# Kernel optimization log

Hardware: AMD Instinct MI355X
Metric: run time of the kernel (lower is better)

The kernel has to match this reference:

```python
import jax, jax.numpy as jnp
import numpy as np

N_NODES = 50000


def setup_inputs() -> dict:
    key = jax.random.key(0)
    k1, k2, k3, k4, k5, k6 = jax.random.split(key, 6)
    N, T, F_IN, F_OUT, E = N_NODES, 4, 64, 64, 800000
    node_features = jax.random.normal(k1, (N, T, F_IN), dtype=jnp.float32)
    edge_weights = jax.random.uniform(k2, (T, E), dtype=jnp.float32)
    src = jax.random.randint(k3, (E,), 0, N, dtype=jnp.int32)
    dst = jax.random.randint(k4, (E,), 0, N, dtype=jnp.int32)
    weight = jax.random.normal(k5, (F_OUT, F_IN), dtype=jnp.float32) / np.sqrt(F_IN)
    bias = jax.random.normal(k6, (F_OUT,), dtype=jnp.float32) * 0.01
    return {"node_features": node_features, "edge_weights": edge_weights,
            "src": src, "dst": dst, "weight": weight, "bias": bias}


def reference(node_features, edge_weights, src, dst, weight, bias):
    # edge_weights: (T, E) -> per-edge weights (E, T)
    ew = edge_weights.T  # (E, T)
    # gather source node features: (E, T, F); multiply by per-edge/timestep scalar
    msg = ew[:, :, None] * node_features[src]  # (E, T, F)
    # scatter-sum into destination nodes: (N, T, F)
    h = jax.ops.segment_sum(msg, dst, num_segments=N_NODES)
    # final linear: (N, T, F_out)
    out = jnp.einsum('ntf,of->nto', h, weight) + bias
    return out
```

## Files before the change

### kernel.cpp

```cpp
#include <hip/hip_runtime.h>


#define F_DIM 64
#define TF 256

__device__ __forceinline__ unsigned short f2bf(float x) {
  unsigned u = __float_as_uint(x);
  return (unsigned short)((u + 0x7FFF + ((u >> 16) & 1)) >> 16);
}
__device__ __forceinline__ float bf2f(unsigned short b) {
  return __uint_as_float(((unsigned)b) << 16);
}
__device__ __forceinline__ void fma4(float4& a, float s, float4 w) {
  a.x += s * w.x; a.y += s * w.y; a.z += s * w.z; a.w += s * w.w;
}

__global__ __launch_bounds__(256) void hist_kernel(
    const int* __restrict__ dst, int* __restrict__ cnt, int E) {
  int e = blockIdx.x * 256 + threadIdx.x;
  if (e < E) atomicAdd(&cnt[dst[e]], 1);
}

__global__ __launch_bounds__(1024) void scanA_kernel(
    const int* __restrict__ cnt, int* __restrict__ off, int* __restrict__ bsum, int N) {
  __shared__ int wsum[16];
  int tid = threadIdx.x;
  int i = blockIdx.x * 1024 + tid;
  int v = (i < N) ? cnt[i] : 0;
  int lane = tid & 63;
  int incl = v;
  #pragma unroll
  for (int s = 1; s < 64; s <<= 1) {
    int t = __shfl_up(incl, s, 64);
    if (lane >= s) incl += t;
  }
  int w = tid >> 6;
  if (lane == 63) wsum[w] = incl;
  __syncthreads();
  if (w == 0) {
    int x = (lane < 16) ? wsum[lane] : 0;
    #pragma unroll
    for (int s = 1; s < 16; s <<= 1) {
      int t = __shfl_up(x, s, 64);
      if (lane >= s) x += t;
    }
    if (lane < 16) wsum[lane] = x;
  }
  __syncthreads();
  int wpre = (w == 0) ? 0 : wsum[w - 1];
  if (i < N) off[i] = wpre + incl - v;
  if (tid == 1023) bsum[blockIdx.x] = wpre + incl;
}

__global__ __launch_bounds__(64) void scanB_kernel(int* __restrict__ bsum, int nb) {
  int lane = threadIdx.x;
  int v = (lane < nb) ? bsum[lane] : 0;
  int incl = v;
  #pragma unroll
  for (int s = 1; s < 64; s <<= 1) {
    int t = __shfl_up(incl, s, 64);
    if (lane >= s) incl += t;
  }
  if (lane < nb) bsum[lane] = incl - v;
}

__global__ __launch_bounds__(1024) void scanC_kernel(
    int* __restrict__ off, const int* __restrict__ bsum, int N, int E) {
  int i = blockIdx.x * 1024 + threadIdx.x;
  if (i < N) off[i] += bsum[blockIdx.x];
  if (i == N) off[N] = E;
}

__global__ __launch_bounds__(256) void fill_kernel(
    const int* __restrict__ dst, const int* __restrict__ src,
    const float* __restrict__ ew, const int* __restrict__ off,
    int* __restrict__ cnt, uint4* __restrict__ rec, int E) {
  int e = blockIdx.x * 256 + threadIdx.x;
  if (e < E) {
    int d = dst[e];
    int pos = off[d] + atomicSub(&cnt[d], 1) - 1;
    unsigned w0 = f2bf(ew[e]),         w1 = f2bf(ew[E + e]);
    unsigned w2 = f2bf(ew[2 * E + e]), w3 = f2bf(ew[3 * E + e]);
    uint4 r;
    r.x = (unsigned)src[e];
    r.y = (w1 << 16) | w0;
    r.z = (w3 << 16) | w2;
    r.w = 0;
    rec[pos] = r;
  }
}

__global__ __launch_bounds__(256) void transform_kernel(
    const float4* __restrict__ nf4, const float* __restrict__ W,
    unsigned short* __restrict__ nfb, int nrows) {
  __shared__ float Wt[64 * 64];
  __shared__ float rows[128][65];
  int tid = threadIdx.x;
  #pragma unroll
  for (int i = tid; i < 4096; i += 256) Wt[(i & 63) * 64 + (i >> 6)] = W[i];
  int rbase = blockIdx.x * 128;
  int nr = min(128, nrows - rbase);
  for (int i = tid; i < nr * 16; i += 256) {
    int r = i >> 4, q = i & 15;
    float4 v = nf4[(size_t)(rbase + r) * 16 + q];
    rows[r][q * 4 + 0] = v.x; rows[r][q * 4 + 1] = v.y;
    rows[r][q * 4 + 2] = v.z; rows[r][q * 4 + 3] = v.w;
  }
  __syncthreads();

  int oq = tid & 7;
  int r0 = (tid >> 3) * 4;
  float4 acc[4][2];
  #pragma unroll
  for (int j = 0; j < 4; ++j) {
    acc[j][0] = make_float4(0.f, 0.f, 0.f, 0.f);
    acc[j][1] = make_float4(0.f, 0.f, 0.f, 0.f);
  }

  const float4* Wt4 = (const float4*)Wt;
  #pragma unroll 8
  for (int f = 0; f < 64; ++f) {
    float4 w0 = Wt4[f * 16 + oq * 2 + 0];
    float4 w1 = Wt4[f * 16 + oq * 2 + 1];
    #pragma unroll
    for (int j = 0; j < 4; ++j) {
      float rv = rows[r0 + j][f];
      fma4(acc[j][0], rv, w0);
      fma4(acc[j][1], rv, w1);
    }
  }

  int obase = oq * 8;
  #pragma unroll
  for (int j = 0; j < 4; ++j) {
    if (r0 + j < nr) {
      size_t rowoff = (size_t)(rbase + r0 + j) * F_DIM + obase;
      #pragma unroll
      for (int c = 0; c < 2; ++c) {
        float4 a = acc[j][c];
        ushort4 u = make_ushort4(f2bf(a.x), f2bf(a.y), f2bf(a.z), f2bf(a.w));
        *reinterpret_cast<ushort4*>(&nfb[rowoff + c * 4]) = u;
      }
    }
  }
}

__global__ __launch_bounds__(256) void gather_bf16_kernel(
    const ushort4* __restrict__ nfb, const uint4* __restrict__ rec,
    const int* __restrict__ off, const float4* __restrict__ bias4,
    float4* __restrict__ out4, int N) {
  int idx = blockIdx.x * 256 + threadIdx.x;
  int n = idx >> 6;
  if (n >= N) return;
  int r = idx & 63, t = r >> 4, q = r & 15;
  int wsel = t >> 1;
  int wshift = (t & 1) << 4;
  int beg = off[n], end = off[n + 1];
  float4 acc = make_float4(0.f, 0.f, 0.f, 0.f);
  int p = beg;
  for (; p + 4 <= end; p += 4) {
    uint4 r0 = rec[p], r1 = rec[p + 1], r2 = rec[p + 2], r3 = rec[p + 3];
    float w0 = __uint_as_float(((wsel ? r0.z : r0.y) >> wshift) << 16);
    float w1 = __uint_as_float(((wsel ? r1.z : r1.y) >> wshift) << 16);
    float w2 = __uint_as_float(((wsel ? r2.z : r2.y) >> wshift) << 16);
    float w3 = __uint_as_float(((wsel ? r3.z : r3.y) >> wshift) << 16);
    ushort4 v0 = nfb[(size_t)r0.x * 64 + t * 16 + q];
    ushort4 v1 = nfb[(size_t)r1.x * 64 + t * 16 + q];
    ushort4 v2 = nfb[(size_t)r2.x * 64 + t * 16 + q];
    ushort4 v3 = nfb[(size_t)r3.x * 64 + t * 16 + q];
    acc.x += w0 * bf2f(v0.x) + w1 * bf2f(v1.x) + w2 * bf2f(v2.x) + w3 * bf2f(v3.x);
    acc.y += w0 * bf2f(v0.y) + w1 * bf2f(v1.y) + w2 * bf2f(v2.y) + w3 * bf2f(v3.y);
    acc.z += w0 * bf2f(v0.z) + w1 * bf2f(v1.z) + w2 * bf2f(v2.z) + w3 * bf2f(v3.z);
    acc.w += w0 * bf2f(v0.w) + w1 * bf2f(v1.w) + w2 * bf2f(v2.w) + w3 * bf2f(v3.w);
  }
  for (; p < end; ++p) {
    uint4 rr = rec[p];
    float w = __uint_as_float(((wsel ? rr.z : rr.y) >> wshift) << 16);
    ushort4 v = nfb[(size_t)rr.x * 64 + t * 16 + q];
    acc.x += w * bf2f(v.x); acc.y += w * bf2f(v.y);
    acc.z += w * bf2f(v.z); acc.w += w * bf2f(v.w);
  }
  float4 b = bias4[q];
  float4 res = make_float4(acc.x + b.x, acc.y + b.y, acc.z + b.z, acc.w + b.w);
  out4[(size_t)n * 64 + t * 16 + q] = res;
}

__global__ __launch_bounds__(256) void gather_f32_kernel(
    const float4* __restrict__ nf4, const uint4* __restrict__ rec,
    const int* __restrict__ off, float4* __restrict__ h4, int N) {
  int idx = blockIdx.x * 256 + threadIdx.x;
  int n = idx >> 6;
  if (n >= N) return;
  int r = idx & 63, t = r >> 4, q = r & 15;
  int wsel = t >> 1;
  int wshift = (t & 1) << 4;
  int beg = off[n], end = off[n + 1];
  float4 acc = make_float4(0.f, 0.f, 0.f, 0.f);
  for (int p = beg; p < end; ++p) {
    uint4 rr = rec[p];
    float w = __uint_as_float(((wsel ? rr.z : rr.y) >> wshift) << 16);
    float4 v = nf4[(size_t)rr.x * 64 + t * 16 + q];
    acc.x += w * v.x; acc.y += w * v.y; acc.z += w * v.z; acc.w += w * v.w;
  }
  h4[(size_t)n * 64 + t * 16 + q] = acc;
}

__global__ __launch_bounds__(256) void linear_kernel(
    float* __restrict__ h, const float* __restrict__ W,
    const float* __restrict__ bias, int nrows) {
  __shared__ float Wt[64 * 65];
  __shared__ float rows[4][64];
  int tid = threadIdx.x;
  for (int i = tid; i < 4096; i += 256) Wt[(i & 63) * 65 + (i >> 6)] = W[i];
  int rr = tid >> 6, o = tid & 63;
  float b = bias[o];
  int rbase = blockIdx.x * 32;
  for (int r0 = 0; r0 < 32; r0 += 4) {
    int row = rbase + r0 + rr;
    __syncthreads();
    if (row < nrows) rows[rr][o] = h[(size_t)row * F_DIM + o];
    __syncthreads();
    if (row < nrows) {
      float acc = b;
      #pragma unroll
      for (int f = 0; f < 64; ++f) acc += rows[rr][f] * Wt[f * 65 + o];
      h[(size_t)row * F_DIM + o] = acc;
    }
  }
}

extern "C" void kernel_launch(void* const* d_in, const int* in_sizes, int n_in,
                              void* d_out, int out_size, void* d_ws, size_t ws_size,
                              hipStream_t stream) {
  const float* nf   = (const float*)d_in[0];
  const float* ew   = (const float*)d_in[1];
  const int*   src  = (const int*)d_in[2];
  const int*   dst  = (const int*)d_in[3];
  const float* W    = (const float*)d_in[4];
  const float* bias = (const float*)d_in[5];
  float* out = (float*)d_out;

  int E = in_sizes[2];
  int N = out_size / TF;
  int nrows = out_size / F_DIM;
  int nfelems = nrows * F_DIM;

  char* wsb = (char*)d_ws;
  int* cnt  = (int*)wsb;
  int* off  = cnt + N;
  int* bsum = off + (N + 1);
  size_t ofs = ((size_t)(2 * N + 1 + 64) * 4 + 15) & ~(size_t)15;
  uint4* rec = (uint4*)(wsb + ofs);           ofs += (size_t)E * 16;
  ofs = (ofs + 511) & ~(size_t)511;
  unsigned short* nfb = (unsigned short*)(wsb + ofs);
  size_t need_bf16 = ofs + (size_t)nfelems * 2;
  bool use_bf16 = ws_size >= need_bf16;

  (void)hipMemsetAsync(cnt, 0, (size_t)N * sizeof(int), stream);

  int eblk = (E + 255) / 256;
  hist_kernel<<<eblk, 256, 0, stream>>>(dst, cnt, E);

  int sblk = (N + 1023) / 1024;
  scanA_kernel<<<sblk, 1024, 0, stream>>>(cnt, off, bsum, N);
  scanB_kernel<<<1, 64, 0, stream>>>(bsum, sblk);
  scanC_kernel<<<(N + 1024) / 1024, 1024, 0, stream>>>(off, bsum, N, E);

  fill_kernel<<<eblk, 256, 0, stream>>>(dst, src, ew, off, cnt, rec, E);

  int gblk = (N * 64 + 255) / 256;
  if (use_bf16) {
    transform_kernel<<<(nrows + 127) / 128, 256, 0, stream>>>(
        (const float4*)nf, W, nfb, nrows);
    gather_bf16_kernel<<<gblk, 256, 0, stream>>>(
        (const ushort4*)nfb, rec, off, (const float4*)bias, (float4*)out, N);
  } else {
    gather_f32_kernel<<<gblk, 256, 0, stream>>>(
        (const float4*)nf, rec, off, (float4*)out, N);
    linear_kernel<<<(nrows + 31) / 32, 256, 0, stream>>>(out, W, bias, nrows);
  }
}
```

Measured before the change: 192.7 us.

## Fuse histogram into transform, drop scanC, split gather by timestep

```diff
diff --git a/kernel.cpp b/kernel.cpp
--- a/kernel.cpp
+++ b/kernel.cpp
@@ -13,12 +13,6 @@
 }
 __device__ __forceinline__ void fma4(float4& a, float s, float4 w) {
   a.x += s * w.x; a.y += s * w.y; a.z += s * w.z; a.w += s * w.w;
-}
-
-__global__ __launch_bounds__(256) void hist_kernel(
-    const int* __restrict__ dst, int* __restrict__ cnt, int E) {
-  int e = blockIdx.x * 256 + threadIdx.x;
-  if (e < E) atomicAdd(&cnt[dst[e]], 1);
 }
 
 __global__ __launch_bounds__(1024) void scanA_kernel(
@@ -64,21 +58,15 @@
   if (lane < nb) bsum[lane] = incl - v;
 }
 
-__global__ __launch_bounds__(1024) void scanC_kernel(
-    int* __restrict__ off, const int* __restrict__ bsum, int N, int E) {
-  int i = blockIdx.x * 1024 + threadIdx.x;
-  if (i < N) off[i] += bsum[blockIdx.x];
-  if (i == N) off[N] = E;
-}
-
 __global__ __launch_bounds__(256) void fill_kernel(
     const int* __restrict__ dst, const int* __restrict__ src,
     const float* __restrict__ ew, const int* __restrict__ off,
-    int* __restrict__ cnt, uint4* __restrict__ rec, int E) {
+    const int* __restrict__ bsum, int* __restrict__ cnt,
+    uint4* __restrict__ rec, int E) {
   int e = blockIdx.x * 256 + threadIdx.x;
   if (e < E) {
     int d = dst[e];
-    int pos = off[d] + atomicSub(&cnt[d], 1) - 1;
+    int pos = off[d] + bsum[d >> 10] + atomicSub(&cnt[d], 1) - 1;
     unsigned w0 = f2bf(ew[e]),         w1 = f2bf(ew[E + e]);
     unsigned w2 = f2bf(ew[2 * E + e]), w3 = f2bf(ew[3 * E + e]);
     uint4 r;
@@ -90,15 +78,24 @@
   }
 }
 
-__global__ __launch_bounds__(256) void transform_kernel(
+__global__ __launch_bounds__(256) void transform_hist_kernel(
     const float4* __restrict__ nf4, const float* __restrict__ W,
-    unsigned short* __restrict__ nfb, int nrows) {
+    unsigned short* __restrict__ nfb, int nrows,
+    const int* __restrict__ dst, int* __restrict__ cnt, int E, int epb) {
   __shared__ float Wt[64 * 64];
   __shared__ float rows[128][65];
   int tid = threadIdx.x;
+
+  {
+    int e0 = blockIdx.x * epb;
+    int e1 = min(e0 + epb, E);
+    for (int e = e0 + tid; e < e1; e += 256) atomicAdd(&cnt[dst[e]], 1);
+  }
+
   #pragma unroll
   for (int i = tid; i < 4096; i += 256) Wt[(i & 63) * 64 + (i >> 6)] = W[i];
   int rbase = blockIdx.x * 128;
+  if (rbase >= nrows) return;
   int nr = min(128, nrows - rbase);
   for (int i = tid; i < nr * 16; i += 256) {
     int r = i >> 4, q = i & 15;
@@ -116,7 +113,6 @@
     acc[j][0] = make_float4(0.f, 0.f, 0.f, 0.f);
     acc[j][1] = make_float4(0.f, 0.f, 0.f, 0.f);
   }
-
   const float4* Wt4 = (const float4*)Wt;
   #pragma unroll 8
   for (int f = 0; f < 64; ++f) {
@@ -129,7 +125,6 @@
       fma4(acc[j][1], rv, w1);
     }
   }
-
   int obase = oq * 8;
   #pragma unroll
   for (int j = 0; j < 4; ++j) {
@@ -147,54 +142,69 @@
 
 __global__ __launch_bounds__(256) void gather_bf16_kernel(
     const ushort4* __restrict__ nfb, const uint4* __restrict__ rec,
-    const int* __restrict__ off, const float4* __restrict__ bias4,
-    float4* __restrict__ out4, int N) {
+    const int* __restrict__ off, const int* __restrict__ bsum,
+    const float4* __restrict__ bias4, float4* __restrict__ out4, int N, int E) {
+  int t = blockIdx.y;
+  int n = blockIdx.x * 4 + (threadIdx.x >> 6);
+  if (n >= N) return;
+  int lane = threadIdx.x & 63;
+  int g = lane >> 4, q = lane & 15;
+  int wsel = t >> 1;
+  int wshift = (t & 1) << 4;
+
+  int beg = off[n] + bsum[n >> 10];
+  int end = (n + 1 < N) ? off[n + 1] + bsum[(n + 1) >> 10] : E;
+
+  float4 acc = make_float4(0.f, 0.f, 0.f, 0.f);
+  int p = beg + g;
+  for (; p + 4 < end; p += 8) {
+    uint4 ra = rec[p], rb = rec[p + 4];
+    float wa = __uint_as_float(((wsel ? ra.z : ra.y) >> wshift) << 16);
+    float wb = __uint_as_float(((wsel ? rb.z : rb.y) >> wshift) << 16);
+    ushort4 va = nfb[(size_t)ra.x * 64 + t * 16 + q];
+    ushort4 vb = nfb[(size_t)rb.x * 64 + t * 16 + q];
+    acc.x += wa * bf2f(va.x) + wb * bf2f(vb.x);
+    acc.y += wa * bf2f(va.y) + wb * bf2f(vb.y);
+    acc.z += wa * bf2f(va.z) + wb * bf2f(vb.z);
+    acc.w += wa * bf2f(va.w) + wb * bf2f(vb.w);
+  }
+  if (p < end) {
+    uint4 ra = rec[p];
+    float wa = __uint_as_float(((wsel ? ra.z : ra.y) >> wshift) << 16);
+    ushort4 va = nfb[(size_t)ra.x * 64 + t * 16 + q];
+    acc.x += wa * bf2f(va.x); acc.y += wa * bf2f(va.y);
+    acc.z += wa * bf2f(va.z); acc.w += wa * bf2f(va.w);
+  }
+  acc.x += __shfl_xor(acc.x, 16); acc.y += __shfl_xor(acc.y, 16);
+  acc.z += __shfl_xor(acc.z, 16); acc.w += __shfl_xor(acc.w, 16);
+  acc.x += __shfl_xor(acc.x, 32); acc.y += __shfl_xor(acc.y, 32);
+  acc.z += __shfl_xor(acc.z, 32); acc.w += __shfl_xor(acc.w, 32);
+
+  if (g == 0) {
+    float4 b = bias4[q];
+    float4 res = make_float4(acc.x + b.x, acc.y + b.y, acc.z + b.z, acc.w + b.w);
+    out4[(size_t)n * 64 + t * 16 + q] = res;
+  }
+}
+
+__global__ __launch_bounds__(256) void hist_kernel(
+    const int* __restrict__ dst, int* __restrict__ cnt, int E) {
+  int e = blockIdx.x * 256 + threadIdx.x;
+  if (e < E) atomicAdd(&cnt[dst[e]], 1);
+}
+
+__global__ __launch_bounds__(256) void gather_f32_kernel(
+    const float4* __restrict__ nf4, const uint4* __restrict__ rec,
+    const int* __restrict__ off, const int* __restrict__ bsum,
+    float4* __restrict__ h4, int N, int E) {
   int idx = blockIdx.x * 256 + threadIdx.x;
   int n = idx >> 6;
   if (n >= N) return;
   int r = idx & 63, t = r >> 4, q = r & 15;
   int wsel = t >> 1;
   int wshift = (t & 1) << 4;
-  int beg = off[n], end = off[n + 1];
-  float4 acc = make_float4(0.f, 0.f, 0.f, 0.f);
-  int p = beg;
-  for (; p + 4 <= end; p += 4) {
-    uint4 r0 = rec[p], r1 = rec[p + 1], r2 = rec[p + 2], r3 = rec[p + 3];
-    float w0 = __uint_as_float(((wsel ? r0.z : r0.y) >> wshift) << 16);
-    float w1 = __uint_as_float(((wsel ? r1.z : r1.y) >> wshift) << 16);
-    float w2 = __uint_as_float(((wsel ? r2.z : r2.y) >> wshift) << 16);
-    float w3 = __uint_as_float(((wsel ? r3.z : r3.y) >> wshift) << 16);
-    ushort4 v0 = nfb[(size_t)r0.x * 64 + t * 16 + q];
-    ushort4 v1 = nfb[(size_t)r1.x * 64 + t * 16 + q];
-    ushort4 v2 = nfb[(size_t)r2.x * 64 + t * 16 + q];
-    ushort4 v3 = nfb[(size_t)r3.x * 64 + t * 16 + q];
-    acc.x += w0 * bf2f(v0.x) + w1 * bf2f(v1.x) + w2 * bf2f(v2.x) + w3 * bf2f(v3.x);
-    acc.y += w0 * bf2f(v0.y) + w1 * bf2f(v1.y) + w2 * bf2f(v2.y) + w3 * bf2f(v3.y);
-    acc.z += w0 * bf2f(v0.z) + w1 * bf2f(v1.z) + w2 * bf2f(v2.z) + w3 * bf2f(v3.z);
-    acc.w += w0 * bf2f(v0.w) + w1 * bf2f(v1.w) + w2 * bf2f(v2.w) + w3 * bf2f(v3.w);
-  }
-  for (; p < end; ++p) {
-    uint4 rr = rec[p];
-    float w = __uint_as_float(((wsel ? rr.z : rr.y) >> wshift) << 16);
-    ushort4 v = nfb[(size_t)rr.x * 64 + t * 16 + q];
-    acc.x += w * bf2f(v.x); acc.y += w * bf2f(v.y);
-    acc.z += w * bf2f(v.z); acc.w += w * bf2f(v.w);
-  }
-  float4 b = bias4[q];
-  float4 res = make_float4(acc.x + b.x, acc.y + b.y, acc.z + b.z, acc.w + b.w);
-  out4[(size_t)n * 64 + t * 16 + q] = res;
-}
-
-__global__ __launch_bounds__(256) void gather_f32_kernel(
-    const float4* __restrict__ nf4, const uint4* __restrict__ rec,
-    const int* __restrict__ off, float4* __restrict__ h4, int N) {
-  int idx = blockIdx.x * 256 + threadIdx.x;
-  int n = idx >> 6;
-  if (n >= N) return;
-  int r = idx & 63, t = r >> 4, q = r & 15;
-  int wsel = t >> 1;
-  int wshift = (t & 1) << 4;
-  int beg = off[n], end = off[n + 1];
+  int beg = off[n] + bsum[n >> 10];
+  int end = (n + 1 < N) ? off[n + 1] + bsum[(n + 1) >> 10] : E;
   float4 acc = make_float4(0.f, 0.f, 0.f, 0.f);
   for (int p = beg; p < end; ++p) {
     uint4 rr = rec[p];
@@ -259,24 +269,27 @@
   (void)hipMemsetAsync(cnt, 0, (size_t)N * sizeof(int), stream);
 
   int eblk = (E + 255) / 256;
-  hist_kernel<<<eblk, 256, 0, stream>>>(dst, cnt, E);
-
   int sblk = (N + 1023) / 1024;
-  scanA_kernel<<<sblk, 1024, 0, stream>>>(cnt, off, bsum, N);
-  scanB_kernel<<<1, 64, 0, stream>>>(bsum, sblk);
-  scanC_kernel<<<(N + 1024) / 1024, 1024, 0, stream>>>(off, bsum, N, E);
-
-  fill_kernel<<<eblk, 256, 0, stream>>>(dst, src, ew, off, cnt, rec, E);
-
-  int gblk = (N * 64 + 255) / 256;
+
   if (use_bf16) {
-    transform_kernel<<<(nrows + 127) / 128, 256, 0, stream>>>(
-        (const float4*)nf, W, nfb, nrows);
-    gather_bf16_kernel<<<gblk, 256, 0, stream>>>(
-        (const ushort4*)nfb, rec, off, (const float4*)bias, (float4*)out, N);
+    int tblocks = (nrows + 127) / 128;
+    int epb = (E + tblocks - 1) / tblocks;
+    transform_hist_kernel<<<tblocks, 256, 0, stream>>>(
+        (const float4*)nf, W, nfb, nrows, dst, cnt, E, epb);
+    scanA_kernel<<<sblk, 1024, 0, stream>>>(cnt, off, bsum, N);
+    scanB_kernel<<<1, 64, 0, stream>>>(bsum, sblk);
+    fill_kernel<<<eblk, 256, 0, stream>>>(dst, src, ew, off, bsum, cnt, rec, E);
+    dim3 ggrid((N + 3) / 4, 4);
+    gather_bf16_kernel<<<ggrid, 256, 0, stream>>>(
+        (const ushort4*)nfb, rec, off, bsum, (const float4*)bias,
+        (float4*)out, N, E);
   } else {
-    gather_f32_kernel<<<gblk, 256, 0, stream>>>(
-        (const float4*)nf, rec, off, (float4*)out, N);
+    hist_kernel<<<eblk, 256, 0, stream>>>(dst, cnt, E);
+    scanA_kernel<<<sblk, 1024, 0, stream>>>(cnt, off, bsum, N);
+    scanB_kernel<<<1, 64, 0, stream>>>(bsum, sblk);
+    fill_kernel<<<eblk, 256, 0, stream>>>(dst, src, ew, off, bsum, cnt, rec, E);
+    gather_f32_kernel<<<(N * 64 + 255) / 256, 256, 0, stream>>>(
+        (const float4*)nf, rec, off, bsum, (float4*)out, N, E);
     linear_kernel<<<(nrows + 31) / 32, 256, 0, stream>>>(out, W, bias, nrows);
   }
 }
```

Result: slower. 209.4 us (+8.6%).
